# Optimization experiments

Measured on AMD Instinct MI355X. Metric: run time of the kernel, lower is better.

Reference implementation:

```python
import jax, jax.numpy as jnp
import numpy as np

T, B, F, H, W, NH = 128, 256, 128, 512, 16, 8
DK = H // NH
EPS = 1e-5  # torch BatchNorm1d default eps


def _bn(x, g, b):
    # BatchNorm1d training-mode forward: normalize over batch dim with biased var
    m = x.mean(0)
    v = x.var(0)
    return (x - m) * jax.lax.rsqrt(v + EPS) * g + b


def setup_inputs() -> dict:
    key = jax.random.key(0)
    ks = jax.random.split(key, 20)
    s = 1.0 / np.sqrt(H)  # pytorch_default init: uniform(-1/sqrt(H), 1/sqrt(H))
    u = lambda k, shp: jax.random.uniform(k, shp, jnp.float32, -s, s)
    return dict(
        x=jax.random.normal(ks[0], (T, B, F), jnp.float32),
        W_ih=u(ks[1], (F, 4 * H)), b_ih=u(ks[2], (4 * H,)),          # input_to_hidden
        W_hh=u(ks[3], (H, 4 * H)),                                    # hidden_to_hidden (no bias)
        Wq_in=u(ks[4], (F + H, H)), bq_in=u(ks[5], (H,)),             # input_and_hidden_to_query
        Wq=u(ks[6], (H, H)), bq=u(ks[7], (H,)),                       # MHA query proj
        Wk=u(ks[8], (H, H)), bk=u(ks[9], (H,)),                       # MHA key proj
        Wv=u(ks[10], (H, H)), bv=u(ks[11], (H,)),                     # MHA value proj
        Wo=u(ks[12], (H, H)), bo=u(ks[13], (H,)),                     # MHA output proj
        W_ac=u(ks[14], (H, 4 * H)), b_ac=u(ks[15], (4 * H,)),         # attention_to_cell (residual mode)
        g_att=jnp.ones((H,), jnp.float32), be_att=jnp.zeros((H,), jnp.float32),
        g_post=jnp.ones((H,), jnp.float32), be_post=jnp.zeros((H,), jnp.float32),
    )


def reference(x, W_ih, b_ih, W_hh, Wq_in, bq_in, Wq, bq, Wk, bk, Wv, bv, Wo, bo,
              W_ac, b_ac, g_att, be_att, g_post, be_post):
    scale = 1.0 / np.sqrt(DK)

    def step(carry, x_t):
        buf, mask, h, c = carry  # buf: [W,B,H] past cells, mask: [W] valid slots
        # Q = elu(Linear(cat[x, h]))
        ih = jnp.concatenate([x_t, h], -1)                      # [B,F+H]
        q = jax.nn.elu(ih @ Wq_in + bq_in)                      # [B,H]
        # Multi-head attention over past-cell window (K = V = past cells)
        Qh = (q @ Wq + bq).reshape(B, NH, DK)                   # [B,NH,DK]
        K = jax.nn.elu(buf @ Wk + bk).reshape(W, B, NH, DK)     # activation_on_keys_and_values
        V = jax.nn.elu(buf @ Wv + bv).reshape(W, B, NH, DK)
        scores = jnp.einsum('bhd,wbhd->bhw', Qh, K) * scale     # [B,NH,W]
        scores = jnp.where(mask[None, None, :], scores, -1e30)
        attn = jax.nn.softmax(scores, -1)
        ctx = jnp.einsum('bhw,wbhd->bhd', attn, V).reshape(B, H)
        att = _bn(jax.nn.elu(ctx @ Wo + bo), g_att, be_att)     # elu then batch_norm_attention_result
        # residual mode: Wx*x + Wh*h + Wa*a + b (pre-activation BN in source is dead code)
        pre = x_t @ W_ih + b_ih + h @ W_hh + att @ W_ac + b_ac  # [B,4H]
        iv = jnp.tanh(pre[:, :H])
        gates = jax.nn.sigmoid(pre[:, H:])
        f_g, i_g, o_g = gates[:, :H], gates[:, H:2 * H], gates[:, 2 * H:]
        c_new = iv * i_g + c * f_g
        h_new = _bn(o_g * jax.nn.elu(c_new), g_post, be_post)
        # append new cell to window (drop oldest)
        buf = jnp.concatenate([buf[1:], c_new[None]], 0)
        mask = jnp.concatenate([mask[1:], jnp.ones((1,), bool)], 0)
        return (buf, mask, h_new, c_new), h_new

    buf0 = jnp.zeros((W, B, H), x.dtype)
    mask0 = jnp.arange(W) == (W - 1)  # deque starts with one zero (h,c) state
    h0 = jnp.zeros((B, H), x.dtype)
    _, hs = jax.lax.scan(step, (buf0, mask0, h0, h0), x)
    return hs  # [T,B,H]
```

## Files before the change

kernel.cpp:

```cpp
#include <hip/hip_runtime.h>
#include <math.h>


#define T_  128
#define B_  256
#define F_  128
#define H_  512
#define W_  16
#define H4_ 2048
#define EPS_ 1e-5f
#define BH_ (B_*H_)
#define NBLK 256
#define NTHR 512
#define FSTRIDE 32

typedef __attribute__((ext_vector_type(4))) float f4;
typedef __attribute__((ext_vector_type(2))) float f2;
typedef unsigned long long u64;

__device__ __forceinline__ float eluf(float x){ return x > 0.f ? x : expf(x) - 1.f; }
__device__ __forceinline__ float sigf(float x){ return 1.f / (1.f + expf(-x)); }

__device__ __forceinline__ f4 ld_c(const float* p) {
  union { f4 v; u64 q[2]; } u;
  u.q[0] = __hip_atomic_load((const u64*)p,     __ATOMIC_RELAXED, __HIP_MEMORY_SCOPE_AGENT);
  u.q[1] = __hip_atomic_load((const u64*)p + 1, __ATOMIC_RELAXED, __HIP_MEMORY_SCOPE_AGENT);
  return u.v;
}
__device__ __forceinline__ void st_c(float* p, f4 v) {
  union { f4 v; u64 q[2]; } u; u.v = v;
  __hip_atomic_store((u64*)p,     u.q[0], __ATOMIC_RELAXED, __HIP_MEMORY_SCOPE_AGENT);
  __hip_atomic_store((u64*)p + 1, u.q[1], __ATOMIC_RELAXED, __HIP_MEMORY_SCOPE_AGENT);
}
__device__ __forceinline__ float ldf_c(const float* p) {
  unsigned u = __hip_atomic_load((const unsigned*)p, __ATOMIC_RELAXED, __HIP_MEMORY_SCOPE_AGENT);
  return __uint_as_float(u);
}
__device__ __forceinline__ void stf_c(float* p, float v) {
  __hip_atomic_store((unsigned*)p, __float_as_uint(v), __ATOMIC_RELAXED, __HIP_MEMORY_SCOPE_AGENT);
}

struct Params {
  const float *x, *W_ih, *b_ih, *W_hh, *Wq_in, *bq_in, *Wq, *bq, *Wk, *bk,
              *Wv, *bv, *Wo, *bo, *W_ac, *b_ac, *g_att, *be_att, *g_post, *be_post;
  float *out, *c, *q, *Qh, *ctx, *attp, *hv, *pre, *Kbuf, *Vbuf, *stA, *stP;
  unsigned *gen, *arr;
};

__device__ __forceinline__ void gbar(unsigned* arr, unsigned* gen, unsigned g) {
  asm volatile("s_waitcnt vmcnt(0) lgkmcnt(0)" ::: "memory");
  __syncthreads();
  const int tid = threadIdx.x;
  if (tid == 0)
    __hip_atomic_store(&arr[blockIdx.x * FSTRIDE], g, __ATOMIC_RELAXED, __HIP_MEMORY_SCOPE_AGENT);
  if (blockIdx.x == 0) {
    if (tid < NBLK) {
      while (__hip_atomic_load(&arr[tid * FSTRIDE], __ATOMIC_RELAXED, __HIP_MEMORY_SCOPE_AGENT) < g)
        __builtin_amdgcn_s_sleep(1);
    }
    __syncthreads();
    if (tid == 0)
      __hip_atomic_store(gen, g, __ATOMIC_RELAXED, __HIP_MEMORY_SCOPE_AGENT);
  } else {
    if (tid == 0) {
      while (__hip_atomic_load(gen, __ATOMIC_RELAXED, __HIP_MEMORY_SCOPE_AGENT) < g)
        __builtin_amdgcn_s_sleep(1);
    }
  }
  __syncthreads();
}

__device__ __forceinline__ void prepP(const float* stP, const float* gn, const float* be,
                                      float* scl, float* shf, int tid) {
  if (tid < H_) {
    float S  = ldf_c(stP + tid);
    float S2 = ldf_c(stP + H_ + tid);
    float mu  = S * (1.f / B_);
    float var = S2 * (1.f / B_) - mu * mu;
    float sc  = rsqrtf(var + EPS_) * gn[tid];
    scl[tid] = sc; shf[tid] = be[tid] - mu * sc;
  }
}

__device__ __forceinline__ void prepA(const float* stA, const float* gn, const float* be,
                                      float* scl, float* shf, int tid) {
  if (tid < H_) {
    float S  = ldf_c(stA + tid) + ldf_c(stA + 1024 + tid) + ldf_c(stA + 2048 + tid) + ldf_c(stA + 3072 + tid);
    float S2 = ldf_c(stA + 512 + tid) + ldf_c(stA + 1536 + tid) + ldf_c(stA + 2560 + tid) + ldf_c(stA + 3584 + tid);
    float mu  = S * (1.f / B_);
    float var = S2 * (1.f / B_) - mu * mu;
    float sc  = rsqrtf(var + EPS_) * gn[tid];
    scl[tid] = sc; shf[tid] = be[tid] - mu * sc;
  }
}

struct GJ {
  const float* A1; int lda1; int K1; int nrm1; int cg1;
  const float* A2; int lda2; int K2; int nrm2; int cg2;
  const float* W1; const float* W2;
  const float* b1; const float* b2; const float* addm;
  float* out; float* stats;
  int N; int m0; int n0; int doElu;
};

__device__ void gemm_tile(const GJ& J, int tid,
                          float (*As)[64][36], float (*Bs)[32][68],
                          const float* scl, const float* shf) {
  const int arow = tid >> 3, akq = (tid & 7) * 4;
  const int bkk = tid >> 4, bnn = (tid & 15) * 4;
  const int ty = tid >> 4, tx = tid & 15;

  float acc[2][4] = {{0.f,0.f,0.f,0.f},{0.f,0.f,0.f,0.f}};

  f4 am0 = {0.f,0.f,0.f,0.f}, am1 = {0.f,0.f,0.f,0.f};
  if (J.addm) {
    am0 = ld_c(J.addm + (size_t)(J.m0 + ty * 2)     * J.N + J.n0 + tx * 4);
    am1 = ld_c(J.addm + (size_t)(J.m0 + ty * 2 + 1) * J.N + J.n0 + tx * 4);
  }

  int buf = 0;
  for (int s = 0; s < 2; ++s) {
    const float* A = s ? J.A2 : J.A1;
    if (!A) break;
    const float* Wp  = s ? J.W2 : J.W1;
    const int K      = s ? J.K2 : J.K1;
    const int lda    = s ? J.lda2 : J.lda1;
    const int nrm    = s ? J.nrm2 : J.nrm1;
    const int cg     = s ? J.cg2 : J.cg1;
    const int nsl    = K >> 5;

    const float* aBase = A + (size_t)(J.m0 + arow) * lda + akq;
    const float* wBase = Wp + (size_t)bkk * J.N + J.n0 + bnn;
    const size_t wSlab = (size_t)32 * J.N;

    f4 aN1 = cg ? ld_c(aBase) : *(const f4*)aBase;
    f4 aN2 = (nsl > 1) ? (cg ? ld_c(aBase + 32) : *(const f4*)(aBase + 32)) : aN1;
    f4 bN1 = *(const f4*)wBase;

    for (int sl = 0; sl < nsl; ++sl) {
      f4 aCur = aN1; aN1 = aN2;
      f4 bCur = bN1;
      if (sl + 2 < nsl) {
        const float* ap = aBase + (size_t)(sl + 2) * 32;
        aN2 = cg ? ld_c(ap) : *(const f4*)ap;
      }
      if (sl + 1 < nsl) bN1 = *(const f4*)(wBase + (size_t)(sl + 1) * wSlab);
      if (nrm) {
        #pragma unroll
        for (int i = 0; i < 4; ++i) {
          int gk = sl * 32 + akq + i;
          aCur[i] = aCur[i] * scl[gk] + shf[gk];
        }
      }
      *(f4*)&As[buf][arow][akq] = aCur;
      *(f4*)&Bs[buf][bkk][bnn] = bCur;
      __syncthreads();
      #pragma unroll
      for (int k = 0; k < 32; k += 2) {
        f2 a0 = *(const f2*)&As[buf][ty * 2][k];
        f2 a1 = *(const f2*)&As[buf][ty * 2 + 1][k];
        f4 b0 = *(const f4*)&Bs[buf][k][tx * 4];
        f4 b1 = *(const f4*)&Bs[buf][k + 1][tx * 4];
        #pragma unroll
        for (int j = 0; j < 4; ++j) {
          acc[0][j] = fmaf(a0[0], b0[j], acc[0][j]);
          acc[0][j] = fmaf(a0[1], b1[j], acc[0][j]);
          acc[1][j] = fmaf(a1[0], b0[j], acc[1][j]);
          acc[1][j] = fmaf(a1[1], b1[j], acc[1][j]);
        }
      }
      buf ^= 1;
    }
  }

  const int r0 = J.m0 + ty * 2, c0 = J.n0 + tx * 4;
  f4 bias = {0.f, 0.f, 0.f, 0.f};
  if (J.b1) bias += *(const f4*)(J.b1 + c0);
  if (J.b2) bias += *(const f4*)(J.b2 + c0);
  f4 v0, v1;
  #pragma unroll
  for (int j = 0; j < 4; ++j) { v0[j] = acc[0][j] + bias[j]; v1[j] = acc[1][j] + bias[j]; }
  if (J.addm) { v0 += am0; v1 += am1; }
  if (J.doElu) {
    #pragma unroll
    for (int j = 0; j < 4; ++j) { v0[j] = eluf(v0[j]); v1[j] = eluf(v1[j]); }
  }
  st_c(J.out + (size_t)r0 * J.N + c0, v0);
  st_c(J.out + (size_t)(r0 + 1) * J.N + c0, v1);

  if (J.stats) {
    float* Af = (float*)As;
    float* Bf = (float*)Bs;
    __syncthreads();
    #pragma unroll
    for (int j = 0; j < 4; ++j) {
      Af[ty * 64 + tx * 4 + j] = v0[j] + v1[j];
      Bf[ty * 64 + tx * 4 + j] = v0[j] * v0[j] + v1[j] * v1[j];
    }
    __syncthreads();
    if (tid < 64) {
      float S = 0.f, S2 = 0.f;
      #pragma unroll
      for (int y = 0; y < 32; ++y) { S += Af[y * 64 + tid]; S2 += Bf[y * 64 + tid]; }
      const int tm = J.m0 >> 6;
      stf_c(J.stats + tm * 1024 + J.n0 + tid, S);
      stf_c(J.stats + tm * 1024 + 512 + J.n0 + tid, S2);
    }
  }
}

__global__ __launch_bounds__(NTHR, 1) void larnn(Params P) {
  __shared__ float As[2][64][36];
  __shared__ float Bs[2][32][68];
  __shared__ float scl[H_], shf[H_];
  __shared__ float Qs[H_];
  __shared__ float sc_[8][16], aw_[8][16];

  const int bid = blockIdx.x, tid = threadIdx.x;
  unsigned g = 0;

  for (int t = 0; t < T_; ++t) {
    const float* xt = P.x + (size_t)t * B_ * F_;
    const int slot = (t - 1) & 15;

    if (bid < 32) {
      if (t > 0) { prepP(P.stP, P.g_post, P.be_post, scl, shf, tid); __syncthreads(); }
      GJ J = {}; J.A1 = xt; J.lda1 = F_; J.K1 = F_;
      if (t > 0) { J.A2 = P.hv; J.lda2 = H_; J.K2 = H_; J.nrm2 = 1; J.cg2 = 1; }
      J.W1 = P.Wq_in; J.W2 = P.Wq_in + (size_t)F_ * H_;
      J.b1 = P.bq_in; J.out = P.q; J.N = H_;
      J.m0 = (bid >> 3) * 64; J.n0 = (bid & 7) * 64; J.doElu = 1;
      gemm_tile(J, tid, As, Bs, scl, shf);
    } else if (bid < 64) {
      int l = bid - 32;
      GJ J = {}; J.A1 = P.c; J.lda1 = H_; J.K1 = H_; J.cg1 = 1;
      J.W1 = P.Wk; J.b1 = P.bk; J.out = P.Kbuf + (size_t)slot * BH_; J.N = H_;
      J.m0 = (l >> 3) * 64; J.n0 = (l & 7) * 64; J.doElu = 1;
      gemm_tile(J, tid, As, Bs, scl, shf);
    } else if (bid < 96) {
      int l = bid - 64;
      GJ J = {}; J.A1 = P.c; J.lda1 = H_; J.K1 = H_; J.cg1 = 1;
      J.W1 = P.Wv; J.b1 = P.bv; J.out = P.Vbuf + (size_t)slot * BH_; J.N = H_;
      J.m0 = (l >> 3) * 64; J.n0 = (l & 7) * 64; J.doElu = 1;
      gemm_tile(J, tid, As, Bs, scl, shf);
    } else if (bid < 224) {
      if (t > 0) { prepP(P.stP, P.g_post, P.be_post, scl, shf, tid); __syncthreads(); }
      const int ix = bid - 96;
      GJ J = {}; J.A1 = xt; J.lda1 = F_; J.K1 = F_;
      if (t > 0) { J.A2 = P.hv; J.lda2 = H_; J.K2 = H_; J.nrm2 = 1; J.cg2 = 1; }
      J.W1 = P.W_ih; J.W2 = P.W_hh;
      J.b1 = P.b_ih; J.b2 = P.b_ac; J.out = P.pre; J.N = H4_;
      J.m0 = (ix >> 5) * 64; J.n0 = (ix & 31) * 64;
      gemm_tile(J, tid, As, Bs, scl, shf);
    } else if (t > 0) {
      prepP(P.stP, P.g_post, P.be_post, scl, shf, tid);
      __syncthreads();
      const int rb0 = (bid - 224) * 8;
      for (int idx = tid; idx < 1024; idx += NTHR) {
        int r = rb0 + (idx >> 7), cc = (idx & 127) * 4;
        f4 hvv = ld_c(P.hv + (size_t)r * H_ + cc);
        f4 v;
        #pragma unroll
        for (int i = 0; i < 4; ++i) v[i] = hvv[i] * scl[cc + i] + shf[cc + i];
        *(f4*)(P.out + (size_t)(t - 1) * BH_ + (size_t)r * H_ + cc) = v;
      }
    }
    gbar(P.arr, P.gen, ++g);

    if (bid < 32) {
      GJ J = {}; J.A1 = P.q; J.lda1 = H_; J.K1 = H_; J.cg1 = 1;
      J.W1 = P.Wq; J.b1 = P.bq; J.out = P.Qh; J.N = H_;
      J.m0 = (bid >> 3) * 64; J.n0 = (bid & 7) * 64;
      gemm_tile(J, tid, As, Bs, scl, shf);
    }
    gbar(P.arr, P.gen, ++g);

    {
      const int b = bid;
      const int nv = (t + 1 < W_) ? t + 1 : W_;
      if (tid < 128) *(f4*)&Qs[tid * 4] = ld_c(P.Qh + (size_t)b * H_ + tid * 4);
      __syncthreads();
      {
        const int p = tid >> 2, l4 = tid & 3;
        const int hh = p >> 4, w = p & 15;
        if (w < nv) {
          const int sl = (t - 1 - w) & 15;
          const float* kp = P.Kbuf + ((size_t)sl * B_ + b) * H_ + hh * 64 + l4 * 16;
          const float* qp = Qs + hh * 64 + l4 * 16;
          float s = 0.f;
          #pragma unroll
          for (int d = 0; d < 16; d += 4) {
            f4 kv = ld_c(kp + d);
            f4 qv = *(const f4*)(qp + d);
            s = fmaf(kv[0], qv[0], fmaf(kv[1], qv[1], fmaf(kv[2], qv[2], fmaf(kv[3], qv[3], s))));
          }
          s += __shfl_xor(s, 1); s += __shfl_xor(s, 2);
          if (l4 == 0) sc_[hh][w] = s * 0.125f;
        }
      }
      __syncthreads();
      if (tid < 8) {
        float mx = -1e30f;
        for (int w = 0; w < nv; ++w) mx = fmaxf(mx, sc_[tid][w]);
        float ss = 0.f;
        for (int w = 0; w < nv; ++w) { float e = expf(sc_[tid][w] - mx); aw_[tid][w] = e; ss += e; }
        float inv = 1.f / ss;
        for (int w = 0; w < nv; ++w) aw_[tid][w] *= inv;
      }
      __syncthreads();
      {
        const int j = tid, hh = j >> 6;
        float o = 0.f;
        for (int w = 0; w < nv; ++w) {
          const int sl = (t - 1 - w) & 15;
          o = fmaf(aw_[hh][w], ldf_c(P.Vbuf + ((size_t)sl * B_ + b) * H_ + j), o);
        }
        stf_c(P.ctx + (size_t)b * H_ + j, o);
      }
    }
    gbar(P.arr, P.gen, ++g);

    if (bid < 32) {
      GJ J = {}; J.A1 = P.ctx; J.lda1 = H_; J.K1 = H_; J.cg1 = 1;
      J.W1 = P.Wo; J.b1 = P.bo; J.doElu = 1;
      J.out = P.attp; J.stats = P.stA; J.N = H_;
      J.m0 = (bid >> 3) * 64; J.n0 = (bid & 7) * 64;
      gemm_tile(J, tid, As, Bs, scl, shf);
    }
    gbar(P.arr, P.gen, ++g);

    if (bid < 128) {
      prepA(P.stA, P.g_att, P.be_att, scl, shf, tid);
      __syncthreads();
      GJ J = {}; J.A1 = P.attp; J.lda1 = H_; J.K1 = H_; J.cg1 = 1; J.nrm1 = 1;
      J.W1 = P.W_ac; J.addm = P.pre; J.out = P.pre; J.N = H4_;
      J.m0 = (bid >> 5) * 64; J.n0 = (bid & 31) * 64;
      gemm_tile(J, tid, As, Bs, scl, shf);
    }
    gbar(P.arr, P.gen, ++g);

    if (bid < 64) {
      f4* rS = (f4*)As;
      f4* rQ = (f4*)Bs;
      const int sub = tid & 1, r = tid >> 1;
      const int c4 = bid * 8 + sub * 4;
      const size_t rb = (size_t)r * H4_;
      f4 p0 = ld_c(P.pre + rb + c4);
      f4 pf = ld_c(P.pre + rb + c4 + 512);
      f4 pi = ld_c(P.pre + rb + c4 + 1024);
      f4 po = ld_c(P.pre + rb + c4 + 1536);
      const size_t ci = (size_t)r * H_ + c4;
      f4 cold = ld_c(P.c + ci);
      f4 cn, hvv;
      #pragma unroll
      for (int i = 0; i < 4; ++i) {
        float iv = tanhf(p0[i]);
        float fg = sigf(pf[i]), ig = sigf(pi[i]), og = sigf(po[i]);
        cn[i] = iv * ig + cold[i] * fg;
        hvv[i] = og * eluf(cn[i]);
      }
      st_c(P.c + ci, cn);
      st_c(P.hv + ci, hvv);
      rS[sub * 256 + r] = hvv;
      rQ[sub * 256 + r] = hvv * hvv;
      __syncthreads();
      for (int s2 = 128; s2 > 0; s2 >>= 1) {
        if (r < s2) {
          rS[sub * 256 + r] += rS[sub * 256 + r + s2];
          rQ[sub * 256 + r] += rQ[sub * 256 + r + s2];
        }
        __syncthreads();
      }
      if (r == 0) {
        f4 S = rS[sub * 256], Q2 = rQ[sub * 256];
        #pragma unroll
        for (int i = 0; i < 4; ++i) { stf_c(P.stP + c4 + i, S[i]); stf_c(P.stP + 512 + c4 + i, Q2[i]); }
      }
    }
    gbar(P.arr, P.gen, ++g);
  }

  if (bid >= 224) {
    prepP(P.stP, P.g_post, P.be_post, scl, shf, tid);
    __syncthreads();
    const int rb0 = (bid - 224) * 8;
    for (int idx = tid; idx < 1024; idx += NTHR) {
      int r = rb0 + (idx >> 7), cc = (idx & 127) * 4;
      f4 hvv = ld_c(P.hv + (size_t)r * H_ + cc);
      f4 v;
      #pragma unroll
      for (int i = 0; i < 4; ++i) v[i] = hvv[i] * scl[cc + i] + shf[cc + i];
      *(f4*)(P.out + (size_t)127 * BH_ + (size_t)r * H_ + cc) = v;
    }
  }
}

#define SYNC_UINTS (32 + NBLK * FSTRIDE)

__global__ __launch_bounds__(256) void pinit(float* c, unsigned* sync) {
  const int i = blockIdx.x * 256 + threadIdx.x;
  if (i < BH_) c[i] = 0.f;
  if (i < SYNC_UINTS) sync[i] = 0u;
}

extern "C" void kernel_launch(void* const* d_in, const int* in_sizes, int n_in,
                              void* d_out, int out_size, void* d_ws, size_t ws_size,
                              hipStream_t stream) {
  Params P;
  P.x      = (const float*)d_in[0];
  P.W_ih   = (const float*)d_in[1];
  P.b_ih   = (const float*)d_in[2];
  P.W_hh   = (const float*)d_in[3];
  P.Wq_in  = (const float*)d_in[4];
  P.bq_in  = (const float*)d_in[5];
  P.Wq     = (const float*)d_in[6];
  P.bq     = (const float*)d_in[7];
  P.Wk     = (const float*)d_in[8];
  P.bk     = (const float*)d_in[9];
  P.Wv     = (const float*)d_in[10];
  P.bv     = (const float*)d_in[11];
  P.Wo     = (const float*)d_in[12];
  P.bo     = (const float*)d_in[13];
  P.W_ac   = (const float*)d_in[14];
  P.b_ac   = (const float*)d_in[15];
  P.g_att  = (const float*)d_in[16];
  P.be_att = (const float*)d_in[17];
  P.g_post = (const float*)d_in[18];
  P.be_post= (const float*)d_in[19];
  P.out    = (float*)d_out;

  unsigned* sync = (unsigned*)d_ws;
  P.gen = sync;
  P.arr = sync + 32;
  float* fb = (float*)d_ws + SYNC_UINTS;
  P.c    = fb;                 fb += BH_;
  P.q    = fb;                 fb += BH_;
  P.Qh   = fb;                 fb += BH_;
  P.ctx  = fb;                 fb += BH_;
  P.attp = fb;                 fb += BH_;
  P.hv   = fb;                 fb += BH_;
  P.pre  = fb;                 fb += (size_t)B_ * H4_;
  P.Kbuf = fb;                 fb += (size_t)W_ * BH_;
  P.Vbuf = fb;                 fb += (size_t)W_ * BH_;
  P.stA  = fb;                 fb += 4096;
  P.stP  = fb;                 fb += 1024;

  pinit<<<(BH_ + 255) / 256, 256, 0, stream>>>(P.c, sync);
  larnn<<<NBLK, NTHR, 0, stream>>>(P);
}
```

Baseline: 16.06 ms.

## Precompute next-step input projections in idle phase, split Qh GEMM, decentralize barrier

The x-dependent parts of the gate and query projections (x@W_ih, x@Wq_in) for step t+1 are now computed during the otherwise idle Qh phase and kept in double-buffered scratch. The per-step critical-path GEMMs then only need K=512 for the hidden term, adding the precomputed result through a new addm field. The Qh projection is split across 64 blocks as two K=256 halves that are summed in the attention phase. The grid barrier drops the two-level gen flag, and every block now polls all arrival flags directly. This removes one round-trip but adds more polling traffic and extra workspace.

After: 25.16 ms. +56.7%, slower.

```diff
diff --git a/kernel.cpp b/kernel.cpp
--- a/kernel.cpp
+++ b/kernel.cpp
@@ -43,29 +43,19 @@
 struct Params {
   const float *x, *W_ih, *b_ih, *W_hh, *Wq_in, *bq_in, *Wq, *bq, *Wk, *bk,
               *Wv, *bv, *Wo, *bo, *W_ac, *b_ac, *g_att, *be_att, *g_post, *be_post;
-  float *out, *c, *q, *Qh, *ctx, *attp, *hv, *pre, *Kbuf, *Vbuf, *stA, *stP;
-  unsigned *gen, *arr;
+  float *out, *c, *q, *QhA, *QhB, *ctx, *attp, *hv, *pre, *Kbuf, *Vbuf, *stA, *stP;
+  float *preX0, *preX1, *qX0, *qX1;
+  unsigned *arr;
 };
 
-__device__ __forceinline__ void gbar(unsigned* arr, unsigned* gen, unsigned g) {
+__device__ __forceinline__ void gbar(unsigned* arr, unsigned g) {
   asm volatile("s_waitcnt vmcnt(0) lgkmcnt(0)" ::: "memory");
   __syncthreads();
-  const int tid = threadIdx.x;
-  if (tid == 0)
+  if (threadIdx.x == 0)
     __hip_atomic_store(&arr[blockIdx.x * FSTRIDE], g, __ATOMIC_RELAXED, __HIP_MEMORY_SCOPE_AGENT);
-  if (blockIdx.x == 0) {
-    if (tid < NBLK) {
-      while (__hip_atomic_load(&arr[tid * FSTRIDE], __ATOMIC_RELAXED, __HIP_MEMORY_SCOPE_AGENT) < g)
-        __builtin_amdgcn_s_sleep(1);
-    }
-    __syncthreads();
-    if (tid == 0)
-      __hip_atomic_store(gen, g, __ATOMIC_RELAXED, __HIP_MEMORY_SCOPE_AGENT);
-  } else {
-    if (tid == 0) {
-      while (__hip_atomic_load(gen, __ATOMIC_RELAXED, __HIP_MEMORY_SCOPE_AGENT) < g)
-        __builtin_amdgcn_s_sleep(1);
-    }
+  if (threadIdx.x < NBLK) {
+    while (__hip_atomic_load(&arr[threadIdx.x * FSTRIDE], __ATOMIC_RELAXED, __HIP_MEMORY_SCOPE_AGENT) < g)
+      __builtin_amdgcn_s_sleep(1);
   }
   __syncthreads();
 }
@@ -219,16 +209,35 @@
   const int bid = blockIdx.x, tid = threadIdx.x;
   unsigned g = 0;
 
+  if (bid < 128) {
+    GJ J = {}; J.A1 = P.x; J.lda1 = F_; J.K1 = F_;
+    J.W1 = P.W_ih; J.b1 = P.b_ih; J.b2 = P.b_ac;
+    J.out = P.preX0; J.N = H4_;
+    J.m0 = (bid >> 5) * 64; J.n0 = (bid & 31) * 64;
+    gemm_tile(J, tid, As, Bs, scl, shf);
+  } else if (bid < 160) {
+    int l = bid - 128;
+    GJ J = {}; J.A1 = P.x; J.lda1 = F_; J.K1 = F_;
+    J.W1 = P.Wq_in; J.b1 = P.bq_in;
+    J.out = P.qX0; J.N = H_;
+    J.m0 = (l >> 3) * 64; J.n0 = (l & 7) * 64;
+    gemm_tile(J, tid, As, Bs, scl, shf);
+  }
+  gbar(P.arr, ++g);
+
   for (int t = 0; t < T_; ++t) {
-    const float* xt = P.x + (size_t)t * B_ * F_;
     const int slot = (t - 1) & 15;
+    float* preX  = (t & 1) ? P.preX1 : P.preX0;
+    float* qX    = (t & 1) ? P.qX1 : P.qX0;
+    float* preXn = (t & 1) ? P.preX0 : P.preX1;
+    float* qXn   = (t & 1) ? P.qX0 : P.qX1;
 
     if (bid < 32) {
       if (t > 0) { prepP(P.stP, P.g_post, P.be_post, scl, shf, tid); __syncthreads(); }
-      GJ J = {}; J.A1 = xt; J.lda1 = F_; J.K1 = F_;
-      if (t > 0) { J.A2 = P.hv; J.lda2 = H_; J.K2 = H_; J.nrm2 = 1; J.cg2 = 1; }
-      J.W1 = P.Wq_in; J.W2 = P.Wq_in + (size_t)F_ * H_;
-      J.b1 = P.bq_in; J.out = P.q; J.N = H_;
+      GJ J = {};
+      if (t > 0) { J.A1 = P.hv; J.lda1 = H_; J.K1 = H_; J.nrm1 = 1; J.cg1 = 1;
+                   J.W1 = P.Wq_in + (size_t)F_ * H_; }
+      J.addm = qX; J.out = P.q; J.N = H_;
       J.m0 = (bid >> 3) * 64; J.n0 = (bid & 7) * 64; J.doElu = 1;
       gemm_tile(J, tid, As, Bs, scl, shf);
     } else if (bid < 64) {
@@ -246,10 +255,10 @@
     } else if (bid < 224) {
       if (t > 0) { prepP(P.stP, P.g_post, P.be_post, scl, shf, tid); __syncthreads(); }
       const int ix = bid - 96;
-      GJ J = {}; J.A1 = xt; J.lda1 = F_; J.K1 = F_;
-      if (t > 0) { J.A2 = P.hv; J.lda2 = H_; J.K2 = H_; J.nrm2 = 1; J.cg2 = 1; }
-      J.W1 = P.W_ih; J.W2 = P.W_hh;
-      J.b1 = P.b_ih; J.b2 = P.b_ac; J.out = P.pre; J.N = H4_;
+      GJ J = {};
+      if (t > 0) { J.A1 = P.hv; J.lda1 = H_; J.K1 = H_; J.nrm1 = 1; J.cg1 = 1;
+                   J.W1 = P.W_hh; }
+      J.addm = preX; J.out = P.pre; J.N = H4_;
       J.m0 = (ix >> 5) * 64; J.n0 = (ix & 31) * 64;
       gemm_tile(J, tid, As, Bs, scl, shf);
     } else if (t > 0) {
@@ -265,20 +274,44 @@
         *(f4*)(P.out + (size_t)(t - 1) * BH_ + (size_t)r * H_ + cc) = v;
       }
     }
-    gbar(P.arr, P.gen, ++g);
+    gbar(P.arr, ++g);
 
     if (bid < 32) {
-      GJ J = {}; J.A1 = P.q; J.lda1 = H_; J.K1 = H_; J.cg1 = 1;
-      J.W1 = P.Wq; J.b1 = P.bq; J.out = P.Qh; J.N = H_;
+      GJ J = {}; J.A1 = P.q; J.lda1 = H_; J.K1 = 256; J.cg1 = 1;
+      J.W1 = P.Wq; J.b1 = P.bq; J.out = P.QhA; J.N = H_;
       J.m0 = (bid >> 3) * 64; J.n0 = (bid & 7) * 64;
       gemm_tile(J, tid, As, Bs, scl, shf);
-    }
-    gbar(P.arr, P.gen, ++g);
+    } else if (bid < 64) {
+      int l = bid - 32;
+      GJ J = {}; J.A1 = P.q + 256; J.lda1 = H_; J.K1 = 256; J.cg1 = 1;
+      J.W1 = P.Wq + (size_t)256 * H_; J.out = P.QhB; J.N = H_;
+      J.m0 = (l >> 3) * 64; J.n0 = (l & 7) * 64;
+      gemm_tile(J, tid, As, Bs, scl, shf);
+    } else if (bid < 192 && t + 1 < T_) {
+      int l = bid - 64;
+      GJ J = {}; J.A1 = P.x + (size_t)(t + 1) * B_ * F_; J.lda1 = F_; J.K1 = F_;
+      J.W1 = P.W_ih; J.b1 = P.b_ih; J.b2 = P.b_ac;
+      J.out = preXn; J.N = H4_;
+      J.m0 = (l >> 5) * 64; J.n0 = (l & 31) * 64;
+      gemm_tile(J, tid, As, Bs, scl, shf);
+    } else if (bid < 224 && t + 1 < T_) {
+      int l = bid - 192;
+      GJ J = {}; J.A1 = P.x + (size_t)(t + 1) * B_ * F_; J.lda1 = F_; J.K1 = F_;
+      J.W1 = P.Wq_in; J.b1 = P.bq_in;
+      J.out = qXn; J.N = H_;
+      J.m0 = (l >> 3) * 64; J.n0 = (l & 7) * 64;
+      gemm_tile(J, tid, As, Bs, scl, shf);
+    }
+    gbar(P.arr, ++g);
 
     {
       const int b = bid;
       const int nv = (t + 1 < W_) ? t + 1 : W_;
-      if (tid < 128) *(f4*)&Qs[tid * 4] = ld_c(P.Qh + (size_t)b * H_ + tid * 4);
+      if (tid < 128) {
+        f4 qa = ld_c(P.QhA + (size_t)b * H_ + tid * 4);
+        f4 qb = ld_c(P.QhB + (size_t)b * H_ + tid * 4);
+        *(f4*)&Qs[tid * 4] = qa + qb;
+      }
       __syncthreads();
       {
         const int p = tid >> 2, l4 = tid & 3;
@@ -318,7 +351,7 @@
         stf_c(P.ctx + (size_t)b * H_ + j, o);
       }
     }
-    gbar(P.arr, P.gen, ++g);
+    gbar(P.arr, ++g);
 
     if (bid < 32) {
       GJ J = {}; J.A1 = P.ctx; J.lda1 = H_; J.K1 = H_; J.cg1 = 1;
@@ -327,7 +360,7 @@
       J.m0 = (bid >> 3) * 64; J.n0 = (bid & 7) * 64;
       gemm_tile(J, tid, As, Bs, scl, shf);
     }
-    gbar(P.arr, P.gen, ++g);
+    gbar(P.arr, ++g);
 
     if (bid < 128) {
       prepA(P.stA, P.g_att, P.be_att, scl, shf, tid);
@@ -337,7 +370,7 @@
       J.m0 = (bid >> 5) * 64; J.n0 = (bid & 31) * 64;
       gemm_tile(J, tid, As, Bs, scl, shf);
     }
-    gbar(P.arr, P.gen, ++g);
+    gbar(P.arr, ++g);
 
     if (bid < 64) {
       f4* rS = (f4*)As;
@@ -377,7 +410,7 @@
         for (int i = 0; i < 4; ++i) { stf_c(P.stP + c4 + i, S[i]); stf_c(P.stP + 512 + c4 + i, Q2[i]); }
       }
     }
-    gbar(P.arr, P.gen, ++g);
+    gbar(P.arr, ++g);
   }
 
   if (bid >= 224) {
@@ -395,7 +428,7 @@
   }
 }
 
-#define SYNC_UINTS (32 + NBLK * FSTRIDE)
+#define SYNC_UINTS (NBLK * FSTRIDE)
 
 __global__ __launch_bounds__(256) void pinit(float* c, unsigned* sync) {
   const int i = blockIdx.x * 256 + threadIdx.x;
@@ -430,20 +463,24 @@
   P.out    = (float*)d_out;
 
   unsigned* sync = (unsigned*)d_ws;
-  P.gen = sync;
-  P.arr = sync + 32;
+  P.arr = sync;
   float* fb = (float*)d_ws + SYNC_UINTS;
-  P.c    = fb;                 fb += BH_;
-  P.q    = fb;                 fb += BH_;
-  P.Qh   = fb;                 fb += BH_;
-  P.ctx  = fb;                 fb += BH_;
-  P.attp = fb;                 fb += BH_;
-  P.hv   = fb;                 fb += BH_;
-  P.pre  = fb;                 fb += (size_t)B_ * H4_;
-  P.Kbuf = fb;                 fb += (size_t)W_ * BH_;
-  P.Vbuf = fb;                 fb += (size_t)W_ * BH_;
-  P.stA  = fb;                 fb += 4096;
-  P.stP  = fb;                 fb += 1024;
+  P.c     = fb; fb += BH_;
+  P.q     = fb; fb += BH_;
+  P.QhA   = fb; fb += BH_;
+  P.QhB   = fb; fb += BH_;
+  P.ctx   = fb; fb += BH_;
+  P.attp  = fb; fb += BH_;
+  P.hv    = fb; fb += BH_;
+  P.pre   = fb; fb += (size_t)B_ * H4_;
+  P.Kbuf  = fb; fb += (size_t)W_ * BH_;
+  P.Vbuf  = fb; fb += (size_t)W_ * BH_;
+  P.preX0 = fb; fb += (size_t)B_ * H4_;
+  P.preX1 = fb; fb += (size_t)B_ * H4_;
+  P.qX0   = fb; fb += BH_;
+  P.qX1   = fb; fb += BH_;
+  P.stA   = fb; fb += 4096;
+  P.stP   = fb; fb += 1024;
 
   pinit<<<(BH_ + 255) / 256, 256, 0, stream>>>(P.c, sync);
   larnn<<<NBLK, NTHR, 0, stream>>>(P);
```

## Widen GEMM tiles to 64x128 with 4x4 register blocking and transposed A

Applied to the files above, without the earlier changes.

The shared gemm_tile helper moves from 64x64 tiles with 2x4 outputs per thread to 64x128 tiles with 4x4 outputs per thread. A is stored transposed in shared memory so each k step needs one float4 load of A and one of B. This halves the number of blocks assigned to each GEMM phase, which is meant to raise FMA-to-LDS intensity and cut redundant weight loads. The cost is that fewer CUs do GEMM work in each phase, the transposed scalar A stores may cause bank conflicts, and per-thread register use rises.

Measured after the change: 33.64 ms. 109% more time.

```diff
diff --git a/kernel.cpp b/kernel.cpp
--- a/kernel.cpp
+++ b/kernel.cpp
@@ -15,7 +15,6 @@
 #define FSTRIDE 32
 
 typedef __attribute__((ext_vector_type(4))) float f4;
-typedef __attribute__((ext_vector_type(2))) float f2;
 typedef unsigned long long u64;
 
 __device__ __forceinline__ float eluf(float x){ return x > 0.f ? x : expf(x) - 1.f; }
@@ -104,18 +103,21 @@
 };
 
 __device__ void gemm_tile(const GJ& J, int tid,
-                          float (*As)[64][36], float (*Bs)[32][68],
+                          float (*As)[32][68], float (*Bs)[32][132],
                           const float* scl, const float* shf) {
   const int arow = tid >> 3, akq = (tid & 7) * 4;
-  const int bkk = tid >> 4, bnn = (tid & 15) * 4;
-  const int ty = tid >> 4, tx = tid & 15;
-
-  float acc[2][4] = {{0.f,0.f,0.f,0.f},{0.f,0.f,0.f,0.f}};
-
-  f4 am0 = {0.f,0.f,0.f,0.f}, am1 = {0.f,0.f,0.f,0.f};
+  const int bkk = tid >> 5, bnn = (tid & 31) * 4;
+  const int ty = tid >> 5, tx = tid & 31;
+
+  f4 z = {0.f, 0.f, 0.f, 0.f};
+  f4 acc0 = z, acc1 = z, acc2 = z, acc3 = z;
+
+  f4 am0 = z, am1 = z, am2 = z, am3 = z;
   if (J.addm) {
-    am0 = ld_c(J.addm + (size_t)(J.m0 + ty * 2)     * J.N + J.n0 + tx * 4);
-    am1 = ld_c(J.addm + (size_t)(J.m0 + ty * 2 + 1) * J.N + J.n0 + tx * 4);
+    am0 = ld_c(J.addm + (size_t)(J.m0 + ty * 4)     * J.N + J.n0 + tx * 4);
+    am1 = ld_c(J.addm + (size_t)(J.m0 + ty * 4 + 1) * J.N + J.n0 + tx * 4);
+    am2 = ld_c(J.addm + (size_t)(J.m0 + ty * 4 + 2) * J.N + J.n0 + tx * 4);
+    am3 = ld_c(J.addm + (size_t)(J.m0 + ty * 4 + 3) * J.N + J.n0 + tx * 4);
   }
 
   int buf = 0;
@@ -135,16 +137,21 @@
 
     f4 aN1 = cg ? ld_c(aBase) : *(const f4*)aBase;
     f4 aN2 = (nsl > 1) ? (cg ? ld_c(aBase + 32) : *(const f4*)(aBase + 32)) : aN1;
-    f4 bN1 = *(const f4*)wBase;
+    f4 bNa = *(const f4*)wBase;
+    f4 bNb = *(const f4*)(wBase + (size_t)16 * J.N);
 
     for (int sl = 0; sl < nsl; ++sl) {
       f4 aCur = aN1; aN1 = aN2;
-      f4 bCur = bN1;
+      f4 bCa = bNa, bCb = bNb;
       if (sl + 2 < nsl) {
         const float* ap = aBase + (size_t)(sl + 2) * 32;
         aN2 = cg ? ld_c(ap) : *(const f4*)ap;
       }
-      if (sl + 1 < nsl) bN1 = *(const f4*)(wBase + (size_t)(sl + 1) * wSlab);
+      if (sl + 1 < nsl) {
+        const float* wp = wBase + (size_t)(sl + 1) * wSlab;
+        bNa = *(const f4*)wp;
+        bNb = *(const f4*)(wp + (size_t)16 * J.N);
+      }
       if (nrm) {
         #pragma unroll
         for (int i = 0; i < 4; ++i) {
@@ -152,41 +159,44 @@
           aCur[i] = aCur[i] * scl[gk] + shf[gk];
         }
       }
-      *(f4*)&As[buf][arow][akq] = aCur;
-      *(f4*)&Bs[buf][bkk][bnn] = bCur;
-      __syncthreads();
       #pragma unroll
-      for (int k = 0; k < 32; k += 2) {
-        f2 a0 = *(const f2*)&As[buf][ty * 2][k];
-        f2 a1 = *(const f2*)&As[buf][ty * 2 + 1][k];
-        f4 b0 = *(const f4*)&Bs[buf][k][tx * 4];
-        f4 b1 = *(const f4*)&Bs[buf][k + 1][tx * 4];
+      for (int i = 0; i < 4; ++i) As[buf][akq + i][arow] = aCur[i];
+      *(f4*)&Bs[buf][bkk][bnn] = bCa;
+      *(f4*)&Bs[buf][bkk + 16][bnn] = bCb;
+      __syncthreads();
+      #pragma unroll
+      for (int k = 0; k < 32; ++k) {
+        f4 av = *(const f4*)&As[buf][k][ty * 4];
+        f4 bv = *(const f4*)&Bs[buf][k][tx * 4];
         #pragma unroll
         for (int j = 0; j < 4; ++j) {
-          acc[0][j] = fmaf(a0[0], b0[j], acc[0][j]);
-          acc[0][j] = fmaf(a0[1], b1[j], acc[0][j]);
-          acc[1][j] = fmaf(a1[0], b0[j], acc[1][j]);
-          acc[1][j] = fmaf(a1[1], b1[j], acc[1][j]);
+          acc0[j] = fmaf(av[0], bv[j], acc0[j]);
+          acc1[j] = fmaf(av[1], bv[j], acc1[j]);
+          acc2[j] = fmaf(av[2], bv[j], acc2[j]);
+          acc3[j] = fmaf(av[3], bv[j], acc3[j]);
         }
       }
       buf ^= 1;
     }
   }
 
-  const int r0 = J.m0 + ty * 2, c0 = J.n0 + tx * 4;
-  f4 bias = {0.f, 0.f, 0.f, 0.f};
+  const int r0 = J.m0 + ty * 4, c0 = J.n0 + tx * 4;
+  f4 bias = z;
   if (J.b1) bias += *(const f4*)(J.b1 + c0);
   if (J.b2) bias += *(const f4*)(J.b2 + c0);
-  f4 v0, v1;
-  #pragma unroll
-  for (int j = 0; j < 4; ++j) { v0[j] = acc[0][j] + bias[j]; v1[j] = acc[1][j] + bias[j]; }
-  if (J.addm) { v0 += am0; v1 += am1; }
+  f4 v0 = acc0 + bias, v1 = acc1 + bias, v2 = acc2 + bias, v3 = acc3 + bias;
+  if (J.addm) { v0 += am0; v1 += am1; v2 += am2; v3 += am3; }
   if (J.doElu) {
     #pragma unroll
-    for (int j = 0; j < 4; ++j) { v0[j] = eluf(v0[j]); v1[j] = eluf(v1[j]); }
+    for (int j = 0; j < 4; ++j) {
+      v0[j] = eluf(v0[j]); v1[j] = eluf(v1[j]);
+      v2[j] = eluf(v2[j]); v3[j] = eluf(v3[j]);
+    }
   }
   st_c(J.out + (size_t)r0 * J.N + c0, v0);
   st_c(J.out + (size_t)(r0 + 1) * J.N + c0, v1);
+  st_c(J.out + (size_t)(r0 + 2) * J.N + c0, v2);
+  st_c(J.out + (size_t)(r0 + 3) * J.N + c0, v3);
 
   if (J.stats) {
     float* Af = (float*)As;
@@ -194,14 +204,14 @@
     __syncthreads();
     #pragma unroll
     for (int j = 0; j < 4; ++j) {
-      Af[ty * 64 + tx * 4 + j] = v0[j] + v1[j];
-      Bf[ty * 64 + tx * 4 + j] = v0[j] * v0[j] + v1[j] * v1[j];
+      Af[ty * 128 + tx * 4 + j] = v0[j] + v1[j] + v2[j] + v3[j];
+      Bf[ty * 128 + tx * 4 + j] = v0[j]*v0[j] + v1[j]*v1[j] + v2[j]*v2[j] + v3[j]*v3[j];
     }
     __syncthreads();
-    if (tid < 64) {
+    if (tid < 128) {
       float S = 0.f, S2 = 0.f;
       #pragma unroll
-      for (int y = 0; y < 32; ++y) { S += Af[y * 64 + tid]; S2 += Bf[y * 64 + tid]; }
+      for (int y = 0; y < 16; ++y) { S += Af[y * 128 + tid]; S2 += Bf[y * 128 + tid]; }
       const int tm = J.m0 >> 6;
       stf_c(J.stats + tm * 1024 + J.n0 + tid, S);
       stf_c(J.stats + tm * 1024 + 512 + J.n0 + tid, S2);
@@ -210,8 +220,8 @@
 }
 
 __global__ __launch_bounds__(NTHR, 1) void larnn(Params P) {
-  __shared__ float As[2][64][36];
-  __shared__ float Bs[2][32][68];
+  __shared__ float As[2][32][68];
+  __shared__ float Bs[2][32][132];
   __shared__ float scl[H_], shf[H_];
   __shared__ float Qs[H_];
   __shared__ float sc_[8][16], aw_[8][16];
@@ -223,36 +233,36 @@
     const float* xt = P.x + (size_t)t * B_ * F_;
     const int slot = (t - 1) & 15;
 
-    if (bid < 32) {
+    if (bid < 16) {
       if (t > 0) { prepP(P.stP, P.g_post, P.be_post, scl, shf, tid); __syncthreads(); }
       GJ J = {}; J.A1 = xt; J.lda1 = F_; J.K1 = F_;
       if (t > 0) { J.A2 = P.hv; J.lda2 = H_; J.K2 = H_; J.nrm2 = 1; J.cg2 = 1; }
       J.W1 = P.Wq_in; J.W2 = P.Wq_in + (size_t)F_ * H_;
       J.b1 = P.bq_in; J.out = P.q; J.N = H_;
-      J.m0 = (bid >> 3) * 64; J.n0 = (bid & 7) * 64; J.doElu = 1;
-      gemm_tile(J, tid, As, Bs, scl, shf);
-    } else if (bid < 64) {
+      J.m0 = (bid >> 2) * 64; J.n0 = (bid & 3) * 128; J.doElu = 1;
+      gemm_tile(J, tid, As, Bs, scl, shf);
+    } else if (bid < 32) {
+      int l = bid - 16;
+      GJ J = {}; J.A1 = P.c; J.lda1 = H_; J.K1 = H_; J.cg1 = 1;
+      J.W1 = P.Wk; J.b1 = P.bk; J.out = P.Kbuf + (size_t)slot * BH_; J.N = H_;
+      J.m0 = (l >> 2) * 64; J.n0 = (l & 3) * 128; J.doElu = 1;
+      gemm_tile(J, tid, As, Bs, scl, shf);
+    } else if (bid < 48) {
       int l = bid - 32;
       GJ J = {}; J.A1 = P.c; J.lda1 = H_; J.K1 = H_; J.cg1 = 1;
-      J.W1 = P.Wk; J.b1 = P.bk; J.out = P.Kbuf + (size_t)slot * BH_; J.N = H_;
-      J.m0 = (l >> 3) * 64; J.n0 = (l & 7) * 64; J.doElu = 1;
-      gemm_tile(J, tid, As, Bs, scl, shf);
-    } else if (bid < 96) {
-      int l = bid - 64;
-      GJ J = {}; J.A1 = P.c; J.lda1 = H_; J.K1 = H_; J.cg1 = 1;
       J.W1 = P.Wv; J.b1 = P.bv; J.out = P.Vbuf + (size_t)slot * BH_; J.N = H_;
-      J.m0 = (l >> 3) * 64; J.n0 = (l & 7) * 64; J.doElu = 1;
-      gemm_tile(J, tid, As, Bs, scl, shf);
-    } else if (bid < 224) {
+      J.m0 = (l >> 2) * 64; J.n0 = (l & 3) * 128; J.doElu = 1;
+      gemm_tile(J, tid, As, Bs, scl, shf);
+    } else if (bid < 112) {
       if (t > 0) { prepP(P.stP, P.g_post, P.be_post, scl, shf, tid); __syncthreads(); }
-      const int ix = bid - 96;
+      const int ix = bid - 48;
       GJ J = {}; J.A1 = xt; J.lda1 = F_; J.K1 = F_;
       if (t > 0) { J.A2 = P.hv; J.lda2 = H_; J.K2 = H_; J.nrm2 = 1; J.cg2 = 1; }
       J.W1 = P.W_ih; J.W2 = P.W_hh;
       J.b1 = P.b_ih; J.b2 = P.b_ac; J.out = P.pre; J.N = H4_;
-      J.m0 = (ix >> 5) * 64; J.n0 = (ix & 31) * 64;
-      gemm_tile(J, tid, As, Bs, scl, shf);
-    } else if (t > 0) {
+      J.m0 = (ix >> 4) * 64; J.n0 = (ix & 15) * 128;
+      gemm_tile(J, tid, As, Bs, scl, shf);
+    } else if (bid >= 224 && t > 0) {
       prepP(P.stP, P.g_post, P.be_post, scl, shf, tid);
       __syncthreads();
       const int rb0 = (bid - 224) * 8;
@@ -267,10 +277,10 @@
     }
     gbar(P.arr, P.gen, ++g);
 
-    if (bid < 32) {
+    if (bid < 16) {
       GJ J = {}; J.A1 = P.q; J.lda1 = H_; J.K1 = H_; J.cg1 = 1;
       J.W1 = P.Wq; J.b1 = P.bq; J.out = P.Qh; J.N = H_;
-      J.m0 = (bid >> 3) * 64; J.n0 = (bid & 7) * 64;
+      J.m0 = (bid >> 2) * 64; J.n0 = (bid & 3) * 128;
       gemm_tile(J, tid, As, Bs, scl, shf);
     }
     gbar(P.arr, P.gen, ++g);
@@ -320,21 +330,21 @@
     }
     gbar(P.arr, P.gen, ++g);
 
-    if (bid < 32) {
+    if (bid < 16) {
       GJ J = {}; J.A1 = P.ctx; J.lda1 = H_; J.K1 = H_; J.cg1 = 1;
       J.W1 = P.Wo; J.b1 = P.bo; J.doElu = 1;
       J.out = P.attp; J.stats = P.stA; J.N = H_;
-      J.m0 = (bid >> 3) * 64; J.n0 = (bid & 7) * 64;
-      gemm_tile(J, tid, As, Bs, scl, shf);
-    }
-    gbar(P.arr, P.gen, ++g);
-
-    if (bid < 128) {
+      J.m0 = (bid >> 2) * 64; J.n0 = (bid & 3) * 128;
+      gemm_tile(J, tid, As, Bs, scl, shf);
+    }
+    gbar(P.arr, P.gen, ++g);
+
+    if (bid < 64) {
       prepA(P.stA, P.g_att, P.be_att, scl, shf, tid);
       __syncthreads();
       GJ J = {}; J.A1 = P.attp; J.lda1 = H_; J.K1 = H_; J.cg1 = 1; J.nrm1 = 1;
       J.W1 = P.W_ac; J.addm = P.pre; J.out = P.pre; J.N = H4_;
-      J.m0 = (bid >> 5) * 64; J.n0 = (bid & 31) * 64;
+      J.m0 = (bid >> 4) * 64; J.n0 = (bid & 15) * 128;
       gemm_tile(J, tid, As, Bs, scl, shf);
     }
     gbar(P.arr, P.gen, ++g);
```

## Double persistent grid to 512 blocks with narrower 64x32 GEMM tiles

Applied to the files above, without the earlier changes.

Raises the persistent cooperative grid from 256 to 512 blocks and halves each GEMM tile's N width from 64 to 32, so every per-step GEMM phase is spread over twice as many blocks. The block-to-work mapping for each phase is rewritten to match, and the launch bound now requests 4 blocks per CU so the larger grid can stay co-resident. The aim is more parallelism in the latency-bound recurrent steps. In exchange each grid barrier must sync twice as many blocks, per-thread work per tile drops, and B-tile reuse falls.

Result: no change. 15.84 ms, median of 2 (-1.4%).

```diff
diff --git a/kernel.cpp b/kernel.cpp
--- a/kernel.cpp
+++ b/kernel.cpp
@@ -10,7 +10,7 @@
 #define H4_ 2048
 #define EPS_ 1e-5f
 #define BH_ (B_*H_)
-#define NBLK 256
+#define NBLK 512
 #define NTHR 512
 #define FSTRIDE 32
 
@@ -31,6 +31,15 @@
   union { f4 v; u64 q[2]; } u; u.v = v;
   __hip_atomic_store((u64*)p,     u.q[0], __ATOMIC_RELAXED, __HIP_MEMORY_SCOPE_AGENT);
   __hip_atomic_store((u64*)p + 1, u.q[1], __ATOMIC_RELAXED, __HIP_MEMORY_SCOPE_AGENT);
+}
+__device__ __forceinline__ f2 ld2_c(const float* p) {
+  union { u64 q; f2 v; } u;
+  u.q = __hip_atomic_load((const u64*)p, __ATOMIC_RELAXED, __HIP_MEMORY_SCOPE_AGENT);
+  return u.v;
+}
+__device__ __forceinline__ void st2_c(float* p, f2 v) {
+  union { f2 v; u64 q; } u; u.v = v;
+  __hip_atomic_store((u64*)p, u.q, __ATOMIC_RELAXED, __HIP_MEMORY_SCOPE_AGENT);
 }
 __device__ __forceinline__ float ldf_c(const float* p) {
   unsigned u = __hip_atomic_load((const unsigned*)p, __ATOMIC_RELAXED, __HIP_MEMORY_SCOPE_AGENT);
@@ -104,18 +113,18 @@
 };
 
 __device__ void gemm_tile(const GJ& J, int tid,
-                          float (*As)[64][36], float (*Bs)[32][68],
+                          float (*As)[64][36], float (*Bs)[32][36],
                           const float* scl, const float* shf) {
   const int arow = tid >> 3, akq = (tid & 7) * 4;
-  const int bkk = tid >> 4, bnn = (tid & 15) * 4;
+  const int bkk = tid >> 4, bnn = (tid & 15) * 2;
   const int ty = tid >> 4, tx = tid & 15;
 
-  float acc[2][4] = {{0.f,0.f,0.f,0.f},{0.f,0.f,0.f,0.f}};
-
-  f4 am0 = {0.f,0.f,0.f,0.f}, am1 = {0.f,0.f,0.f,0.f};
+  float acc[2][2] = {{0.f,0.f},{0.f,0.f}};
+
+  f2 am0 = {0.f,0.f}, am1 = {0.f,0.f};
   if (J.addm) {
-    am0 = ld_c(J.addm + (size_t)(J.m0 + ty * 2)     * J.N + J.n0 + tx * 4);
-    am1 = ld_c(J.addm + (size_t)(J.m0 + ty * 2 + 1) * J.N + J.n0 + tx * 4);
+    am0 = ld2_c(J.addm + (size_t)(J.m0 + ty * 2)     * J.N + J.n0 + tx * 2);
+    am1 = ld2_c(J.addm + (size_t)(J.m0 + ty * 2 + 1) * J.N + J.n0 + tx * 2);
   }
 
   int buf = 0;
@@ -135,16 +144,16 @@
 
     f4 aN1 = cg ? ld_c(aBase) : *(const f4*)aBase;
     f4 aN2 = (nsl > 1) ? (cg ? ld_c(aBase + 32) : *(const f4*)(aBase + 32)) : aN1;
-    f4 bN1 = *(const f4*)wBase;
+    f2 bN1 = *(const f2*)wBase;
 
     for (int sl = 0; sl < nsl; ++sl) {
       f4 aCur = aN1; aN1 = aN2;
-      f4 bCur = bN1;
+      f2 bCur = bN1;
       if (sl + 2 < nsl) {
         const float* ap = aBase + (size_t)(sl + 2) * 32;
         aN2 = cg ? ld_c(ap) : *(const f4*)ap;
       }
-      if (sl + 1 < nsl) bN1 = *(const f4*)(wBase + (size_t)(sl + 1) * wSlab);
+      if (sl + 1 < nsl) bN1 = *(const f2*)(wBase + (size_t)(sl + 1) * wSlab);
       if (nrm) {
         #pragma unroll
         for (int i = 0; i < 4; ++i) {
@@ -153,55 +162,55 @@
         }
       }
       *(f4*)&As[buf][arow][akq] = aCur;
-      *(f4*)&Bs[buf][bkk][bnn] = bCur;
+      *(f2*)&Bs[buf][bkk][bnn] = bCur;
       __syncthreads();
       #pragma unroll
       for (int k = 0; k < 32; k += 2) {
         f2 a0 = *(const f2*)&As[buf][ty * 2][k];
         f2 a1 = *(const f2*)&As[buf][ty * 2 + 1][k];
-        f4 b0 = *(const f4*)&Bs[buf][k][tx * 4];
-        f4 b1 = *(const f4*)&Bs[buf][k + 1][tx * 4];
-        #pragma unroll
-        for (int j = 0; j < 4; ++j) {
-          acc[0][j] = fmaf(a0[0], b0[j], acc[0][j]);
-          acc[0][j] = fmaf(a0[1], b1[j], acc[0][j]);
-          acc[1][j] = fmaf(a1[0], b0[j], acc[1][j]);
-          acc[1][j] = fmaf(a1[1], b1[j], acc[1][j]);
-        }
+        f2 b0 = *(const f2*)&Bs[buf][k][tx * 2];
+        f2 b1 = *(const f2*)&Bs[buf][k + 1][tx * 2];
+        acc[0][0] = fmaf(a0[0], b0[0], acc[0][0]);
+        acc[0][1] = fmaf(a0[0], b0[1], acc[0][1]);
+        acc[0][0] = fmaf(a0[1], b1[0], acc[0][0]);
+        acc[0][1] = fmaf(a0[1], b1[1], acc[0][1]);
+        acc[1][0] = fmaf(a1[0], b0[0], acc[1][0]);
+        acc[1][1] = fmaf(a1[0], b0[1], acc[1][1]);
+        acc[1][0] = fmaf(a1[1], b1[0], acc[1][0]);
+        acc[1][1] = fmaf(a1[1], b1[1], acc[1][1]);
       }
       buf ^= 1;
     }
   }
 
-  const int r0 = J.m0 + ty * 2, c0 = J.n0 + tx * 4;
-  f4 bias = {0.f, 0.f, 0.f, 0.f};
-  if (J.b1) bias += *(const f4*)(J.b1 + c0);
-  if (J.b2) bias += *(const f4*)(J.b2 + c0);
-  f4 v0, v1;
-  #pragma unroll
-  for (int j = 0; j < 4; ++j) { v0[j] = acc[0][j] + bias[j]; v1[j] = acc[1][j] + bias[j]; }
+  const int r0 = J.m0 + ty * 2, c0 = J.n0 + tx * 2;
+  f2 bias = {0.f, 0.f};
+  if (J.b1) bias += *(const f2*)(J.b1 + c0);
+  if (J.b2) bias += *(const f2*)(J.b2 + c0);
+  f2 v0, v1;
+  v0[0] = acc[0][0] + bias[0]; v0[1] = acc[0][1] + bias[1];
+  v1[0] = acc[1][0] + bias[0]; v1[1] = acc[1][1] + bias[1];
   if (J.addm) { v0 += am0; v1 += am1; }
   if (J.doElu) {
-    #pragma unroll
-    for (int j = 0; j < 4; ++j) { v0[j] = eluf(v0[j]); v1[j] = eluf(v1[j]); }
-  }
-  st_c(J.out + (size_t)r0 * J.N + c0, v0);
-  st_c(J.out + (size_t)(r0 + 1) * J.N + c0, v1);
+    v0[0] = eluf(v0[0]); v0[1] = eluf(v0[1]);
+    v1[0] = eluf(v1[0]); v1[1] = eluf(v1[1]);
+  }
+  st2_c(J.out + (size_t)r0 * J.N + c0, v0);
+  st2_c(J.out + (size_t)(r0 + 1) * J.N + c0, v1);
 
   if (J.stats) {
     float* Af = (float*)As;
     float* Bf = (float*)Bs;
     __syncthreads();
-    #pragma unroll
-    for (int j = 0; j < 4; ++j) {
-      Af[ty * 64 + tx * 4 + j] = v0[j] + v1[j];
-      Bf[ty * 64 + tx * 4 + j] = v0[j] * v0[j] + v1[j] * v1[j];
-    }
+    Af[ty * 32 + tx * 2]     = v0[0] + v1[0];
+    Af[ty * 32 + tx * 2 + 1] = v0[1] + v1[1];
+    Bf[ty * 32 + tx * 2]     = v0[0] * v0[0] + v1[0] * v1[0];
+    Bf[ty * 32 + tx * 2 + 1] = v0[1] * v0[1] + v1[1] * v1[1];
     __syncthreads();
-    if (tid < 64) {
+    if (tid < 32) {
       float S = 0.f, S2 = 0.f;
       #pragma unroll
-      for (int y = 0; y < 32; ++y) { S += Af[y * 64 + tid]; S2 += Bf[y * 64 + tid]; }
+      for (int y = 0; y < 32; ++y) { S += Af[y * 32 + tid]; S2 += Bf[y * 32 + tid]; }
       const int tm = J.m0 >> 6;
       stf_c(J.stats + tm * 1024 + J.n0 + tid, S);
       stf_c(J.stats + tm * 1024 + 512 + J.n0 + tid, S2);
@@ -209,9 +218,9 @@
   }
 }
 
-__global__ __launch_bounds__(NTHR, 1) void larnn(Params P) {
+__global__ __launch_bounds__(NTHR, 4) void larnn(Params P) {
   __shared__ float As[2][64][36];
-  __shared__ float Bs[2][32][68];
+  __shared__ float Bs[2][32][36];
   __shared__ float scl[H_], shf[H_];
   __shared__ float Qs[H_];
   __shared__ float sc_[8][16], aw_[8][16];
@@ -223,39 +232,39 @@
     const float* xt = P.x + (size_t)t * B_ * F_;
     const int slot = (t - 1) & 15;
 
-    if (bid < 32) {
+    if (bid < 64) {
       if (t > 0) { prepP(P.stP, P.g_post, P.be_post, scl, shf, tid); __syncthreads(); }
       GJ J = {}; J.A1 = xt; J.lda1 = F_; J.K1 = F_;
       if (t > 0) { J.A2 = P.hv; J.lda2 = H_; J.K2 = H_; J.nrm2 = 1; J.cg2 = 1; }
       J.W1 = P.Wq_in; J.W2 = P.Wq_in + (size_t)F_ * H_;
       J.b1 = P.bq_in; J.out = P.q; J.N = H_;
-      J.m0 = (bid >> 3) * 64; J.n0 = (bid & 7) * 64; J.doElu = 1;
-      gemm_tile(J, tid, As, Bs, scl, shf);
-    } else if (bid < 64) {
-      int l = bid - 32;
+      J.m0 = (bid >> 4) * 64; J.n0 = (bid & 15) * 32; J.doElu = 1;
+      gemm_tile(J, tid, As, Bs, scl, shf);
+    } else if (bid < 128) {
+      int l = bid - 64;
       GJ J = {}; J.A1 = P.c; J.lda1 = H_; J.K1 = H_; J.cg1 = 1;
       J.W1 = P.Wk; J.b1 = P.bk; J.out = P.Kbuf + (size_t)slot * BH_; J.N = H_;
-      J.m0 = (l >> 3) * 64; J.n0 = (l & 7) * 64; J.doElu = 1;
-      gemm_tile(J, tid, As, Bs, scl, shf);
-    } else if (bid < 96) {
-      int l = bid - 64;
+      J.m0 = (l >> 4) * 64; J.n0 = (l & 15) * 32; J.doElu = 1;
+      gemm_tile(J, tid, As, Bs, scl, shf);
+    } else if (bid < 192) {
+      int l = bid - 128;
       GJ J = {}; J.A1 = P.c; J.lda1 = H_; J.K1 = H_; J.cg1 = 1;
       J.W1 = P.Wv; J.b1 = P.bv; J.out = P.Vbuf + (size_t)slot * BH_; J.N = H_;
-      J.m0 = (l >> 3) * 64; J.n0 = (l & 7) * 64; J.doElu = 1;
-      gemm_tile(J, tid, As, Bs, scl, shf);
-    } else if (bid < 224) {
+      J.m0 = (l >> 4) * 64; J.n0 = (l & 15) * 32; J.doElu = 1;
+      gemm_tile(J, tid, As, Bs, scl, shf);
+    } else if (bid < 448) {
       if (t > 0) { prepP(P.stP, P.g_post, P.be_post, scl, shf, tid); __syncthreads(); }
-      const int ix = bid - 96;
+      const int ix = bid - 192;
       GJ J = {}; J.A1 = xt; J.lda1 = F_; J.K1 = F_;
       if (t > 0) { J.A2 = P.hv; J.lda2 = H_; J.K2 = H_; J.nrm2 = 1; J.cg2 = 1; }
       J.W1 = P.W_ih; J.W2 = P.W_hh;
       J.b1 = P.b_ih; J.b2 = P.b_ac; J.out = P.pre; J.N = H4_;
-      J.m0 = (ix >> 5) * 64; J.n0 = (ix & 31) * 64;
-      gemm_tile(J, tid, As, Bs, scl, shf);
-    } else if (t > 0) {
+      J.m0 = (ix >> 6) * 64; J.n0 = (ix & 63) * 32;
+      gemm_tile(J, tid, As, Bs, scl, shf);
+    } else if (bid < 480 && t > 0) {
       prepP(P.stP, P.g_post, P.be_post, scl, shf, tid);
       __syncthreads();
-      const int rb0 = (bid - 224) * 8;
+      const int rb0 = (bid - 448) * 8;
       for (int idx = tid; idx < 1024; idx += NTHR) {
         int r = rb0 + (idx >> 7), cc = (idx & 127) * 4;
         f4 hvv = ld_c(P.hv + (size_t)r * H_ + cc);
@@ -267,15 +276,15 @@
     }
     gbar(P.arr, P.gen, ++g);
 
-    if (bid < 32) {
+    if (bid < 64) {
       GJ J = {}; J.A1 = P.q; J.lda1 = H_; J.K1 = H_; J.cg1 = 1;
       J.W1 = P.Wq; J.b1 = P.bq; J.out = P.Qh; J.N = H_;
-      J.m0 = (bid >> 3) * 64; J.n0 = (bid & 7) * 64;
-      gemm_tile(J, tid, As, Bs, scl, shf);
-    }
-    gbar(P.arr, P.gen, ++g);
-
-    {
+      J.m0 = (bid >> 4) * 64; J.n0 = (bid & 15) * 32;
+      gemm_tile(J, tid, As, Bs, scl, shf);
+    }
+    gbar(P.arr, P.gen, ++g);
+
+    if (bid < B_) {
       const int b = bid;
       const int nv = (t + 1 < W_) ? t + 1 : W_;
       if (tid < 128) *(f4*)&Qs[tid * 4] = ld_c(P.Qh + (size_t)b * H_ + tid * 4);
@@ -320,21 +329,21 @@
     }
     gbar(P.arr, P.gen, ++g);
 
-    if (bid < 32) {
+    if (bid < 64) {
       GJ J = {}; J.A1 = P.ctx; J.lda1 = H_; J.K1 = H_; J.cg1 = 1;
       J.W1 = P.Wo; J.b1 = P.bo; J.doElu = 1;
       J.out = P.attp; J.stats = P.stA; J.N = H_;
-      J.m0 = (bid >> 3) * 64; J.n0 = (bid & 7) * 64;
-      gemm_tile(J, tid, As, Bs, scl, shf);
-    }
-    gbar(P.arr, P.gen, ++g);
-
-    if (bid < 128) {
+      J.m0 = (bid >> 4) * 64; J.n0 = (bid & 15) * 32;
+      gemm_tile(J, tid, As, Bs, scl, shf);
+    }
+    gbar(P.arr, P.gen, ++g);
+
+    if (bid < 256) {
       prepA(P.stA, P.g_att, P.be_att, scl, shf, tid);
       __syncthreads();
       GJ J = {}; J.A1 = P.attp; J.lda1 = H_; J.K1 = H_; J.cg1 = 1; J.nrm1 = 1;
       J.W1 = P.W_ac; J.addm = P.pre; J.out = P.pre; J.N = H4_;
-      J.m0 = (bid >> 5) * 64; J.n0 = (bid & 31) * 64;
+      J.m0 = (bid >> 6) * 64; J.n0 = (bid & 63) * 32;
       gemm_tile(J, tid, As, Bs, scl, shf);
     }
     gbar(P.arr, P.gen, ++g);
@@ -380,10 +389,10 @@
     gbar(P.arr, P.gen, ++g);
   }
 
-  if (bid >= 224) {
+  if (bid >= 448 && bid < 480) {
     prepP(P.stP, P.g_post, P.be_post, scl, shf, tid);
     __syncthreads();
-    const int rb0 = (bid - 224) * 8;
+    const int rb0 = (bid - 448) * 8;
     for (int idx = tid; idx < 1024; idx += NTHR) {
       int r = rb0 + (idx >> 7), cc = (idx & 127) * 4;
       f4 hvv = ld_c(P.hv + (size_t)r * H_ + cc);
```
